# Kernel optimization log

Hardware: AMD Instinct MI355X
Metric: run time of the kernel (lower is better)

The kernel has to match this reference:

```python
import jax, jax.numpy as jnp
import numpy as np

K = 512
N = 65536
BN_EPS = 1e-5


def setup_inputs() -> dict:
    key = jax.random.key(0)
    kx, = jax.random.split(key, 1)
    X = jax.random.normal(kx, (N, K), dtype=jnp.float32)
    C1 = jnp.eye(K, dtype=jnp.float32)
    C2 = jnp.ones((K,), dtype=jnp.float32)
    C3 = jnp.zeros((1,), dtype=jnp.float32)
    return {"X": X, "C1": C1, "C2": C2, "C3": C3}


def reference(X, C1, C2, C3):
    # diag(X @ C1 @ X.T) == sum((X @ C1) * X, axis=-1)  (row-wise quadratic form)
    quad = jnp.einsum("nk,kj,nj->n", X, C1, X)  # [N]
    y = quad[:, None] + C2 * X + C3              # [N, K]
    # BatchNorm1d (training mode, affine=False): biased batch stats per feature
    mean = jnp.mean(y, axis=0)
    var = jnp.mean((y - mean) ** 2, axis=0)
    return (y - mean) / jnp.sqrt(var + BN_EPS)
```

## Files before the change

kernel.cpp:

```cpp
#include <hip/hip_runtime.h>

#define NROWS 65536
#define KDIM  512
constexpr float BN_EPS = 1e-5f;

using short8 = __attribute__((ext_vector_type(8))) short;
using f32x4  = __attribute__((ext_vector_type(4))) float;

#define BM 128

__device__ __forceinline__ void gload_lds16(const void* g, void* l) {
  __builtin_amdgcn_global_load_lds(
      (const __attribute__((address_space(1))) void*)g,
      (__attribute__((address_space(3))) void*)l, 16, 0, 0);
}

__device__ __forceinline__ short8 cvthi8(const float4& a, const float4& b) {
  const float e[8] = {a.x, a.y, a.z, a.w, b.x, b.y, b.z, b.w};
  short8 h;
  #pragma unroll
  for (int i = 0; i < 8; ++i) {
    unsigned u = __float_as_uint(e[i]);
    u += 0x7FFFu + ((u >> 16) & 1u);
    h[i] = (short)(u >> 16);
  }
  return h;
}

__global__ __launch_bounds__(256)
void prep_c1(const float* __restrict__ C1, short8* __restrict__ c1tH) {
  const int e   = blockIdx.x * 256 + threadIdx.x;
  const int col = e & 511;
  const int kg  = e >> 9;
  short8 hi;
  #pragma unroll
  for (int i = 0; i < 8; ++i) {
    const float x = C1[(size_t)(kg * 8 + i) * KDIM + col];
    unsigned u = __float_as_uint(x);
    u += 0x7FFFu + ((u >> 16) & 1u);
    hi[i] = (short)(u >> 16);
  }
  c1tH[e] = hi;
}

__global__ __launch_bounds__(1024)
void quad_kernel(const float* __restrict__ X, const short8* __restrict__ c1tH,
                 float* __restrict__ quad,
                 float* __restrict__ colS1, float* __restrict__ colS2,
                 float* __restrict__ colS3, double* __restrict__ qsums) {
  __shared__ short8 Bs[3][2048];
  __shared__ float  As[3][4096];
  __shared__ float qPart[4][BM];
  __shared__ float qLds[BM];

  const int tid  = threadIdx.x;
  const int lane = tid & 63;
  const int w    = tid >> 6;
  const int wr   = w >> 2;
  const int wc   = w & 3;
  const int g    = lane >> 4;
  const int lr   = lane & 15;
  const int r0   = blockIdx.x * BM;

  const int arow = tid >> 3;
  const int ac   = tid & 7;
  const float* asrc = X + (size_t)(r0 + arow) * KDIM + ((ac ^ (arow & 7)) * 4);

#define STAGE(bufi, kt)                                                    \
  {                                                                        \
    gload_lds16(c1tH + (kt) * 2048 + tid,        &Bs[bufi][tid]);          \
    gload_lds16(c1tH + (kt) * 2048 + 1024 + tid, &Bs[bufi][1024 + tid]);   \
    gload_lds16(asrc + (kt) * 32,                &As[bufi][tid * 4]);      \
  }

  f32x4 acc[2][8];
  #pragma unroll
  for (int rf = 0; rf < 2; ++rf)
    #pragma unroll
    for (int cf = 0; cf < 8; ++cf)
      acc[rf][cf] = (f32x4){0.f, 0.f, 0.f, 0.f};

  STAGE(0, 0);
  STAGE(1, 1);
  asm volatile("s_waitcnt vmcnt(3)" ::: "memory");
  __builtin_amdgcn_s_barrier();
  __builtin_amdgcn_sched_barrier(0);

  #pragma unroll
  for (int kt = 0; kt < 16; ++kt) {
    const int buf = kt % 3;
    if (kt < 14) STAGE((kt + 2) % 3, kt + 2);
    short8 A0, A1;
    {
      const int row0 = wr * 32 + lr;
      const float4 a00 = *(const float4*)&As[buf][row0 * 32 + (((2 * g) ^ (row0 & 7)) * 4)];
      const float4 a01 = *(const float4*)&As[buf][row0 * 32 + (((2 * g + 1) ^ (row0 & 7)) * 4)];
      A0 = cvthi8(a00, a01);
      const int row1 = row0 + 16;
      const float4 a10 = *(const float4*)&As[buf][row1 * 32 + (((2 * g) ^ (row1 & 7)) * 4)];
      const float4 a11 = *(const float4*)&As[buf][row1 * 32 + (((2 * g + 1) ^ (row1 & 7)) * 4)];
      A1 = cvthi8(a10, a11);
    }
    const int fb = g * 512 + wc * 128 + lr;
    {
      const short8 b0 = Bs[buf][fb];
      const short8 b1 = Bs[buf][fb + 16];
      const short8 b2 = Bs[buf][fb + 32];
      const short8 b3 = Bs[buf][fb + 48];
      acc[0][0] = __builtin_amdgcn_mfma_f32_16x16x32_bf16(A0, b0, acc[0][0], 0, 0, 0);
      acc[1][0] = __builtin_amdgcn_mfma_f32_16x16x32_bf16(A1, b0, acc[1][0], 0, 0, 0);
      acc[0][1] = __builtin_amdgcn_mfma_f32_16x16x32_bf16(A0, b1, acc[0][1], 0, 0, 0);
      acc[1][1] = __builtin_amdgcn_mfma_f32_16x16x32_bf16(A1, b1, acc[1][1], 0, 0, 0);
      acc[0][2] = __builtin_amdgcn_mfma_f32_16x16x32_bf16(A0, b2, acc[0][2], 0, 0, 0);
      acc[1][2] = __builtin_amdgcn_mfma_f32_16x16x32_bf16(A1, b2, acc[1][2], 0, 0, 0);
      acc[0][3] = __builtin_amdgcn_mfma_f32_16x16x32_bf16(A0, b3, acc[0][3], 0, 0, 0);
      acc[1][3] = __builtin_amdgcn_mfma_f32_16x16x32_bf16(A1, b3, acc[1][3], 0, 0, 0);
    }
    {
      const short8 b4 = Bs[buf][fb + 64];
      const short8 b5 = Bs[buf][fb + 80];
      const short8 b6 = Bs[buf][fb + 96];
      const short8 b7 = Bs[buf][fb + 112];
      acc[0][4] = __builtin_amdgcn_mfma_f32_16x16x32_bf16(A0, b4, acc[0][4], 0, 0, 0);
      acc[1][4] = __builtin_amdgcn_mfma_f32_16x16x32_bf16(A1, b4, acc[1][4], 0, 0, 0);
      acc[0][5] = __builtin_amdgcn_mfma_f32_16x16x32_bf16(A0, b5, acc[0][5], 0, 0, 0);
      acc[1][5] = __builtin_amdgcn_mfma_f32_16x16x32_bf16(A1, b5, acc[1][5], 0, 0, 0);
      acc[0][6] = __builtin_amdgcn_mfma_f32_16x16x32_bf16(A0, b6, acc[0][6], 0, 0, 0);
      acc[1][6] = __builtin_amdgcn_mfma_f32_16x16x32_bf16(A1, b6, acc[1][6], 0, 0, 0);
      acc[0][7] = __builtin_amdgcn_mfma_f32_16x16x32_bf16(A0, b7, acc[0][7], 0, 0, 0);
      acc[1][7] = __builtin_amdgcn_mfma_f32_16x16x32_bf16(A1, b7, acc[1][7], 0, 0, 0);
    }
    if (kt < 14) {
      asm volatile("s_waitcnt vmcnt(3)" ::: "memory");
    } else if (kt == 14) {
      asm volatile("s_waitcnt vmcnt(0)" ::: "memory");
    }
    if (kt < 15) {
      __builtin_amdgcn_s_barrier();
      __builtin_amdgcn_sched_barrier(0);
    }
  }
#undef STAGE

  #pragma unroll
  for (int rf = 0; rf < 2; ++rf)
    #pragma unroll
    for (int p = 0; p < 4; ++p) {
      const int row = wr * 32 + rf * 16 + g * 4 + p;
      const float* xr = X + (size_t)(r0 + row) * KDIM + wc * 128;
      float s = 0.f;
      #pragma unroll
      for (int cf = 0; cf < 8; ++cf)
        s += acc[rf][cf][p] * xr[cf * 16 + lr];
      s += __shfl_xor(s, 1, 64);
      s += __shfl_xor(s, 2, 64);
      s += __shfl_xor(s, 4, 64);
      s += __shfl_xor(s, 8, 64);
      if (lr == 0) qPart[wc][row] = s;
    }
  __syncthreads();
  if (tid < BM) {
    const float q = qPart[0][tid] + qPart[1][tid] + qPart[2][tid] + qPart[3][tid];
    quad[r0 + tid] = q;
    qLds[tid] = q;
  }
  __syncthreads();
  {
    const int col   = tid & 511;
    const int rbase = (tid >> 9) * 64;
    float s1 = 0.f, s2 = 0.f, s3 = 0.f;
    for (int r = rbase; r < rbase + 64; ++r) {
      const float q = qLds[r];
      const float x = X[(size_t)(r0 + r) * KDIM + col];
      s1 += x; s2 += x * x; s3 += q * x;
    }
    atomicAdd(&colS1[col], s1);
    atomicAdd(&colS2[col], s2);
    atomicAdd(&colS3[col], s3);
  }
  if (tid < BM) {
    double q = (double)qLds[tid];
    double q2 = q * q;
    #pragma unroll
    for (int m = 1; m < 64; m <<= 1) {
      q  += __shfl_xor(q,  m, 64);
      q2 += __shfl_xor(q2, m, 64);
    }
    if ((tid & 63) == 0) { atomicAdd(&qsums[0], q); atomicAdd(&qsums[1], q2); }
  }
}

__global__ void finalize_kernel(const float* __restrict__ colS1, const float* __restrict__ colS2,
                                const float* __restrict__ colS3, const double* __restrict__ qsums,
                                const float* __restrict__ C2, const float* __restrict__ C3,
                                float* __restrict__ mean, float* __restrict__ inv_std) {
  const int k = blockIdx.x * blockDim.x + threadIdx.x;
  if (k >= KDIM) return;
  const double invN = 1.0 / (double)NROWS;
  const double meanQ = qsums[0] * invN;
  const double varQ  = qsums[1] * invN - meanQ * meanQ;
  const float meanX = colS1[k] * (float)invN;
  const float varX  = colS2[k] * (float)invN - meanX * meanX;
  const float covQX = colS3[k] * (float)invN - (float)meanQ * meanX;
  const float c2 = C2[k];
  const float c3 = C3[0];
  const float m = (float)meanQ + c2 * meanX + c3;
  const float v = (float)varQ + c2 * c2 * varX + 2.0f * c2 * covQX;
  mean[k] = m;
  inv_std[k] = 1.0f / sqrtf(v + BN_EPS);
}

__global__ __launch_bounds__(256)
void normalize_kernel(const float* __restrict__ X, const float* __restrict__ quad,
                      const float* __restrict__ C2, const float* __restrict__ C3,
                      const float* __restrict__ mean, const float* __restrict__ inv_std,
                      float* __restrict__ out) {
  const int idx = blockIdx.x * blockDim.x + threadIdx.x;
  const int n = idx >> 7;
  const int j4 = idx & 127;
  const float q = quad[n];
  const float c3 = C3[0];
  const float4 x  = *(const float4*)&X[(size_t)idx * 4];
  const float4 c2 = *(const float4*)&C2[j4 * 4];
  const float4 m  = *(const float4*)&mean[j4 * 4];
  const float4 iv = *(const float4*)&inv_std[j4 * 4];
  float4 o;
  o.x = (q + c2.x * x.x + c3 - m.x) * iv.x;
  o.y = (q + c2.y * x.y + c3 - m.y) * iv.y;
  o.z = (q + c2.z * x.z + c3 - m.z) * iv.z;
  o.w = (q + c2.w * x.w + c3 - m.w) * iv.w;
  *(float4*)&out[(size_t)idx * 4] = o;
}

extern "C" void kernel_launch(void* const* d_in, const int* in_sizes, int n_in,
                              void* d_out, int out_size, void* d_ws, size_t ws_size,
                              hipStream_t stream) {
  const float* X  = (const float*)d_in[0];
  const float* C1 = (const float*)d_in[1];
  const float* C2 = (const float*)d_in[2];
  const float* C3 = (const float*)d_in[3];
  float* out = (float*)d_out;

  char* ws = (char*)d_ws;
  float*  quad    = (float*)ws;
  float*  colS1   = (float*)(ws + (size_t)NROWS * 4);
  float*  colS2   = colS1 + KDIM;
  float*  colS3   = colS2 + KDIM;
  double* qsums   = (double*)(ws + (size_t)NROWS * 4 + 3 * KDIM * 4);
  float*  mean    = (float*)(ws + (size_t)NROWS * 4 + 3 * KDIM * 4 + 16);
  float*  inv_std = mean + KDIM;
  short8* c1tH    = (short8*)(ws + 276480);

  hipMemsetAsync(colS1, 0, 3 * KDIM * 4 + 16, stream);

  prep_c1<<<128, 256, 0, stream>>>(C1, c1tH);
  quad_kernel<<<NROWS / BM, 1024, 0, stream>>>(X, c1tH, quad,
                                               colS1, colS2, colS3, qsums);
  finalize_kernel<<<2, 256, 0, stream>>>(colS1, colS2, colS3, qsums, C2, C3, mean, inv_std);
  normalize_kernel<<<(NROWS * (KDIM / 4)) / 256, 256, 0, stream>>>(
      X, quad, C2, C3, mean, inv_std, out);
}
```

Before: 136.5 us.

## Halve quad-kernel block size, give each wave 64 rows, and spread stat atomics

The quad kernel drops from 1024 to 512 threads per block. Each wave now computes four 16-row MFMA fragments instead of two, so every LDS-loaded C1 fragment feeds more MFMAs, and each thread issues six direct-to-LDS loads per stage instead of three. Column-statistic atomics now go to four copies of the accumulators, selected by block index, and the quad-sum atomics go to 32 slots; the finalize kernel adds these partials back together, which cuts contention on the same addresses. The bf16 conversion uses the HIP intrinsic instead of manual rounding. The risk is that the LDS footprint (about 146 KB) still allows only one block per CU, so fewer resident waves are left to hide latency.

```diff
diff --git a/kernel.cpp b/kernel.cpp
--- a/kernel.cpp
+++ b/kernel.cpp
@@ -1,4 +1,5 @@
 #include <hip/hip_runtime.h>
+#include <hip/hip_bf16.h>
 
 #define NROWS 65536
 #define KDIM  512
@@ -15,15 +16,14 @@
       (__attribute__((address_space(3))) void*)l, 16, 0, 0);
 }
 
-__device__ __forceinline__ short8 cvthi8(const float4& a, const float4& b) {
-  const float e[8] = {a.x, a.y, a.z, a.w, b.x, b.y, b.z, b.w};
+__device__ __forceinline__ short bf16bits(float x) {
+  __hip_bfloat16 h = __float2bfloat16(x);
+  return *reinterpret_cast<short*>(&h);
+}
+__device__ __forceinline__ short8 cvt8(const float4& a, const float4& b) {
   short8 h;
-  #pragma unroll
-  for (int i = 0; i < 8; ++i) {
-    unsigned u = __float_as_uint(e[i]);
-    u += 0x7FFFu + ((u >> 16) & 1u);
-    h[i] = (short)(u >> 16);
-  }
+  h[0] = bf16bits(a.x); h[1] = bf16bits(a.y); h[2] = bf16bits(a.z); h[3] = bf16bits(a.w);
+  h[4] = bf16bits(b.x); h[5] = bf16bits(b.y); h[6] = bf16bits(b.z); h[7] = bf16bits(b.w);
   return h;
 }
 
@@ -34,20 +34,16 @@
   const int kg  = e >> 9;
   short8 hi;
   #pragma unroll
-  for (int i = 0; i < 8; ++i) {
-    const float x = C1[(size_t)(kg * 8 + i) * KDIM + col];
-    unsigned u = __float_as_uint(x);
-    u += 0x7FFFu + ((u >> 16) & 1u);
-    hi[i] = (short)(u >> 16);
-  }
+  for (int i = 0; i < 8; ++i)
+    hi[i] = bf16bits(C1[(size_t)(kg * 8 + i) * KDIM + col]);
   c1tH[e] = hi;
 }
 
-__global__ __launch_bounds__(1024)
+__global__ __launch_bounds__(512, 2)
 void quad_kernel(const float* __restrict__ X, const short8* __restrict__ c1tH,
                  float* __restrict__ quad,
                  float* __restrict__ colS1, float* __restrict__ colS2,
-                 float* __restrict__ colS3, double* __restrict__ qsums) {
+                 float* __restrict__ colS3, double* __restrict__ qsumsA) {
   __shared__ short8 Bs[3][2048];
   __shared__ float  As[3][4096];
   __shared__ float qPart[4][BM];
@@ -60,29 +56,34 @@
   const int wc   = w & 3;
   const int g    = lane >> 4;
   const int lr   = lane & 15;
-  const int r0   = blockIdx.x * BM;
+  const int bid  = blockIdx.x;
+  const int r0   = bid * BM;
 
   const int arow = tid >> 3;
   const int ac   = tid & 7;
-  const float* asrc = X + (size_t)(r0 + arow) * KDIM + ((ac ^ (arow & 7)) * 4);
+  const float* asrc0 = X + (size_t)(r0 + arow) * KDIM + ((ac ^ (arow & 7)) * 4);
+  const float* asrc1 = asrc0 + (size_t)64 * KDIM;
 
 #define STAGE(bufi, kt)                                                    \
   {                                                                        \
     gload_lds16(c1tH + (kt) * 2048 + tid,        &Bs[bufi][tid]);          \
+    gload_lds16(c1tH + (kt) * 2048 + 512 + tid,  &Bs[bufi][512 + tid]);    \
     gload_lds16(c1tH + (kt) * 2048 + 1024 + tid, &Bs[bufi][1024 + tid]);   \
-    gload_lds16(asrc + (kt) * 32,                &As[bufi][tid * 4]);      \
-  }
-
-  f32x4 acc[2][8];
-  #pragma unroll
-  for (int rf = 0; rf < 2; ++rf)
+    gload_lds16(c1tH + (kt) * 2048 + 1536 + tid, &Bs[bufi][1536 + tid]);   \
+    gload_lds16(asrc0 + (kt) * 32, &As[bufi][tid * 4]);                    \
+    gload_lds16(asrc1 + (kt) * 32, &As[bufi][(512 + tid) * 4]);            \
+  }
+
+  f32x4 acc[4][8];
+  #pragma unroll
+  for (int rf = 0; rf < 4; ++rf)
     #pragma unroll
     for (int cf = 0; cf < 8; ++cf)
       acc[rf][cf] = (f32x4){0.f, 0.f, 0.f, 0.f};
 
   STAGE(0, 0);
   STAGE(1, 1);
-  asm volatile("s_waitcnt vmcnt(3)" ::: "memory");
+  asm volatile("s_waitcnt vmcnt(6)" ::: "memory");
   __builtin_amdgcn_s_barrier();
   __builtin_amdgcn_sched_barrier(0);
 
@@ -90,16 +91,13 @@
   for (int kt = 0; kt < 16; ++kt) {
     const int buf = kt % 3;
     if (kt < 14) STAGE((kt + 2) % 3, kt + 2);
-    short8 A0, A1;
-    {
-      const int row0 = wr * 32 + lr;
-      const float4 a00 = *(const float4*)&As[buf][row0 * 32 + (((2 * g) ^ (row0 & 7)) * 4)];
-      const float4 a01 = *(const float4*)&As[buf][row0 * 32 + (((2 * g + 1) ^ (row0 & 7)) * 4)];
-      A0 = cvthi8(a00, a01);
-      const int row1 = row0 + 16;
-      const float4 a10 = *(const float4*)&As[buf][row1 * 32 + (((2 * g) ^ (row1 & 7)) * 4)];
-      const float4 a11 = *(const float4*)&As[buf][row1 * 32 + (((2 * g + 1) ^ (row1 & 7)) * 4)];
-      A1 = cvthi8(a10, a11);
+    short8 Af[4];
+    #pragma unroll
+    for (int rf = 0; rf < 4; ++rf) {
+      const int row = wr * 64 + rf * 16 + lr;
+      const float4 x0 = *(const float4*)&As[buf][row * 32 + (((2 * g) ^ (row & 7)) * 4)];
+      const float4 x1 = *(const float4*)&As[buf][row * 32 + (((2 * g + 1) ^ (row & 7)) * 4)];
+      Af[rf] = cvt8(x0, x1);
     }
     const int fb = g * 512 + wc * 128 + lr;
     {
@@ -107,31 +105,29 @@
       const short8 b1 = Bs[buf][fb + 16];
       const short8 b2 = Bs[buf][fb + 32];
       const short8 b3 = Bs[buf][fb + 48];
-      acc[0][0] = __builtin_amdgcn_mfma_f32_16x16x32_bf16(A0, b0, acc[0][0], 0, 0, 0);
-      acc[1][0] = __builtin_amdgcn_mfma_f32_16x16x32_bf16(A1, b0, acc[1][0], 0, 0, 0);
-      acc[0][1] = __builtin_amdgcn_mfma_f32_16x16x32_bf16(A0, b1, acc[0][1], 0, 0, 0);
-      acc[1][1] = __builtin_amdgcn_mfma_f32_16x16x32_bf16(A1, b1, acc[1][1], 0, 0, 0);
-      acc[0][2] = __builtin_amdgcn_mfma_f32_16x16x32_bf16(A0, b2, acc[0][2], 0, 0, 0);
-      acc[1][2] = __builtin_amdgcn_mfma_f32_16x16x32_bf16(A1, b2, acc[1][2], 0, 0, 0);
-      acc[0][3] = __builtin_amdgcn_mfma_f32_16x16x32_bf16(A0, b3, acc[0][3], 0, 0, 0);
-      acc[1][3] = __builtin_amdgcn_mfma_f32_16x16x32_bf16(A1, b3, acc[1][3], 0, 0, 0);
+      #pragma unroll
+      for (int rf = 0; rf < 4; ++rf) {
+        acc[rf][0] = __builtin_amdgcn_mfma_f32_16x16x32_bf16(Af[rf], b0, acc[rf][0], 0, 0, 0);
+        acc[rf][1] = __builtin_amdgcn_mfma_f32_16x16x32_bf16(Af[rf], b1, acc[rf][1], 0, 0, 0);
+        acc[rf][2] = __builtin_amdgcn_mfma_f32_16x16x32_bf16(Af[rf], b2, acc[rf][2], 0, 0, 0);
+        acc[rf][3] = __builtin_amdgcn_mfma_f32_16x16x32_bf16(Af[rf], b3, acc[rf][3], 0, 0, 0);
+      }
     }
     {
       const short8 b4 = Bs[buf][fb + 64];
       const short8 b5 = Bs[buf][fb + 80];
       const short8 b6 = Bs[buf][fb + 96];
       const short8 b7 = Bs[buf][fb + 112];
-      acc[0][4] = __builtin_amdgcn_mfma_f32_16x16x32_bf16(A0, b4, acc[0][4], 0, 0, 0);
-      acc[1][4] = __builtin_amdgcn_mfma_f32_16x16x32_bf16(A1, b4, acc[1][4], 0, 0, 0);
-      acc[0][5] = __builtin_amdgcn_mfma_f32_16x16x32_bf16(A0, b5, acc[0][5], 0, 0, 0);
-      acc[1][5] = __builtin_amdgcn_mfma_f32_16x16x32_bf16(A1, b5, acc[1][5], 0, 0, 0);
-      acc[0][6] = __builtin_amdgcn_mfma_f32_16x16x32_bf16(A0, b6, acc[0][6], 0, 0, 0);
-      acc[1][6] = __builtin_amdgcn_mfma_f32_16x16x32_bf16(A1, b6, acc[1][6], 0, 0, 0);
-      acc[0][7] = __builtin_amdgcn_mfma_f32_16x16x32_bf16(A0, b7, acc[0][7], 0, 0, 0);
-      acc[1][7] = __builtin_amdgcn_mfma_f32_16x16x32_bf16(A1, b7, acc[1][7], 0, 0, 0);
+      #pragma unroll
+      for (int rf = 0; rf < 4; ++rf) {
+        acc[rf][4] = __builtin_amdgcn_mfma_f32_16x16x32_bf16(Af[rf], b4, acc[rf][4], 0, 0, 0);
+        acc[rf][5] = __builtin_amdgcn_mfma_f32_16x16x32_bf16(Af[rf], b5, acc[rf][5], 0, 0, 0);
+        acc[rf][6] = __builtin_amdgcn_mfma_f32_16x16x32_bf16(Af[rf], b6, acc[rf][6], 0, 0, 0);
+        acc[rf][7] = __builtin_amdgcn_mfma_f32_16x16x32_bf16(Af[rf], b7, acc[rf][7], 0, 0, 0);
+      }
     }
     if (kt < 14) {
-      asm volatile("s_waitcnt vmcnt(3)" ::: "memory");
+      asm volatile("s_waitcnt vmcnt(6)" ::: "memory");
     } else if (kt == 14) {
       asm volatile("s_waitcnt vmcnt(0)" ::: "memory");
     }
@@ -143,10 +139,10 @@
 #undef STAGE
 
   #pragma unroll
-  for (int rf = 0; rf < 2; ++rf)
+  for (int rf = 0; rf < 4; ++rf)
     #pragma unroll
     for (int p = 0; p < 4; ++p) {
-      const int row = wr * 32 + rf * 16 + g * 4 + p;
+      const int row = wr * 64 + rf * 16 + g * 4 + p;
       const float* xr = X + (size_t)(r0 + row) * KDIM + wc * 128;
       float s = 0.f;
       #pragma unroll
@@ -166,17 +162,16 @@
   }
   __syncthreads();
   {
-    const int col   = tid & 511;
-    const int rbase = (tid >> 9) * 64;
+    const int cb = (bid & 3) * 512;
     float s1 = 0.f, s2 = 0.f, s3 = 0.f;
-    for (int r = rbase; r < rbase + 64; ++r) {
+    for (int r = 0; r < BM; ++r) {
       const float q = qLds[r];
-      const float x = X[(size_t)(r0 + r) * KDIM + col];
+      const float x = X[(size_t)(r0 + r) * KDIM + tid];
       s1 += x; s2 += x * x; s3 += q * x;
     }
-    atomicAdd(&colS1[col], s1);
-    atomicAdd(&colS2[col], s2);
-    atomicAdd(&colS3[col], s3);
+    atomicAdd(&colS1[cb + tid], s1);
+    atomicAdd(&colS2[cb + tid], s2);
+    atomicAdd(&colS3[cb + tid], s3);
   }
   if (tid < BM) {
     double q = (double)qLds[tid];
@@ -186,22 +181,34 @@
       q  += __shfl_xor(q,  m, 64);
       q2 += __shfl_xor(q2, m, 64);
     }
-    if ((tid & 63) == 0) { atomicAdd(&qsums[0], q); atomicAdd(&qsums[1], q2); }
+    if ((tid & 63) == 0) {
+      atomicAdd(&qsumsA[(bid & 31) * 2],     q);
+      atomicAdd(&qsumsA[(bid & 31) * 2 + 1], q2);
+    }
   }
 }
 
 __global__ void finalize_kernel(const float* __restrict__ colS1, const float* __restrict__ colS2,
-                                const float* __restrict__ colS3, const double* __restrict__ qsums,
+                                const float* __restrict__ colS3, const double* __restrict__ qsumsA,
                                 const float* __restrict__ C2, const float* __restrict__ C3,
                                 float* __restrict__ mean, float* __restrict__ inv_std) {
+  __shared__ double sQ[2];
+  if (threadIdx.x == 0) {
+    double a = 0.0, b = 0.0;
+    for (int i = 0; i < 32; ++i) { a += qsumsA[2 * i]; b += qsumsA[2 * i + 1]; }
+    sQ[0] = a; sQ[1] = b;
+  }
+  __syncthreads();
   const int k = blockIdx.x * blockDim.x + threadIdx.x;
   if (k >= KDIM) return;
   const double invN = 1.0 / (double)NROWS;
-  const double meanQ = qsums[0] * invN;
-  const double varQ  = qsums[1] * invN - meanQ * meanQ;
-  const float meanX = colS1[k] * (float)invN;
-  const float varX  = colS2[k] * (float)invN - meanX * meanX;
-  const float covQX = colS3[k] * (float)invN - (float)meanQ * meanX;
+  const double meanQ = sQ[0] * invN;
+  const double varQ  = sQ[1] * invN - meanQ * meanQ;
+  const float meanX = (colS1[k] + colS1[k + 512] + colS1[k + 1024] + colS1[k + 1536]) * (float)invN;
+  const float s2    = (colS2[k] + colS2[k + 512] + colS2[k + 1024] + colS2[k + 1536]) * (float)invN;
+  const float s3    = (colS3[k] + colS3[k + 512] + colS3[k + 1024] + colS3[k + 1536]) * (float)invN;
+  const float varX  = s2 - meanX * meanX;
+  const float covQX = s3 - (float)meanQ * meanX;
   const float c2 = C2[k];
   const float c3 = C3[0];
   const float m = (float)meanQ + c2 * meanX + c3;
@@ -243,20 +250,20 @@
 
   char* ws = (char*)d_ws;
   float*  quad    = (float*)ws;
-  float*  colS1   = (float*)(ws + (size_t)NROWS * 4);
-  float*  colS2   = colS1 + KDIM;
-  float*  colS3   = colS2 + KDIM;
-  double* qsums   = (double*)(ws + (size_t)NROWS * 4 + 3 * KDIM * 4);
-  float*  mean    = (float*)(ws + (size_t)NROWS * 4 + 3 * KDIM * 4 + 16);
-  float*  inv_std = mean + KDIM;
-  short8* c1tH    = (short8*)(ws + 276480);
-
-  hipMemsetAsync(colS1, 0, 3 * KDIM * 4 + 16, stream);
+  float*  colS1   = (float*)(ws + 262144);
+  float*  colS2   = (float*)(ws + 262144 + 8192);
+  float*  colS3   = (float*)(ws + 262144 + 16384);
+  double* qsumsA  = (double*)(ws + 262144 + 24576);
+  float*  mean    = (float*)(ws + 262144 + 25088);
+  float*  inv_std = (float*)(ws + 262144 + 27136);
+  short8* c1tH    = (short8*)(ws + 294912);
+
+  hipMemsetAsync(colS1, 0, 24576 + 512, stream);
 
   prep_c1<<<128, 256, 0, stream>>>(C1, c1tH);
-  quad_kernel<<<NROWS / BM, 1024, 0, stream>>>(X, c1tH, quad,
-                                               colS1, colS2, colS3, qsums);
-  finalize_kernel<<<2, 256, 0, stream>>>(colS1, colS2, colS3, qsums, C2, C3, mean, inv_std);
+  quad_kernel<<<NROWS / BM, 512, 0, stream>>>(X, c1tH, quad,
+                                              colS1, colS2, colS3, qsumsA);
+  finalize_kernel<<<2, 256, 0, stream>>>(colS1, colS2, colS3, qsumsA, C2, C3, mean, inv_std);
   normalize_kernel<<<(NROWS * (KDIM / 4)) / 256, 256, 0, stream>>>(
       X, quad, C2, C3, mean, inv_std, out);
 }
```

Result: faster. 120.7 us (-11.6%).
